# Kernel optimization log

Hardware: AMD Instinct MI355X
Metric: run time of the kernel (lower is better)

Reference implementation:

```python
import jax, jax.numpy as jnp
import numpy as np

N_HEADS = 16
EMBD = 1024
D_HEAD = EMBD // N_HEADS

def setup_inputs() -> dict:
    key = jax.random.key(0)
    ks = jax.random.split(key, 5)
    x = jax.random.normal(ks[0], (2, 2048, EMBD), dtype=jnp.float32)
    # Linear weights stored torch-style [out, in]; apply as x @ W.T + b
    W_in = jax.random.normal(ks[1], (3 * EMBD, EMBD), dtype=jnp.float32) * (EMBD ** -0.5)
    b_in = jax.random.normal(ks[2], (3 * EMBD,), dtype=jnp.float32) * 0.01
    W_out = jax.random.normal(ks[3], (EMBD, EMBD), dtype=jnp.float32) * (EMBD ** -0.5)
    b_out = jax.random.normal(ks[4], (EMBD,), dtype=jnp.float32) * 0.01
    return {"x": x, "W_in": W_in, "b_in": b_in, "W_out": W_out, "b_out": b_out}

def reference(x, W_in, b_in, W_out, b_out):
    B, S, D = x.shape
    qkv = x @ W_in.T + b_in                      # [B, S, 3D]
    q, k, v = jnp.split(qkv, 3, axis=-1)
    def heads(t):
        return t.reshape(B, S, N_HEADS, D_HEAD).transpose(0, 2, 1, 3)  # [B,H,S,d]
    q, k, v = heads(q), heads(k), heads(v)
    scale = 1.0 / jnp.sqrt(jnp.float32(D_HEAD))
    scores = jnp.einsum('bhqd,bhkd->bhqk', q, k) * scale
    weights = jax.nn.softmax(scores, axis=-1)
    out = jnp.einsum('bhqk,bhkd->bhqd', weights, v)  # [B,H,S,d]
    out = out.transpose(0, 2, 1, 3).reshape(B, S, D)
    return out @ W_out.T + b_out
```

## Files before the change

### kernel.cpp

```cpp
#include <hip/hip_runtime.h>
#include <cstdint>

#define EMBD 1024
#define NH 16
#define DH 64
#define BB 2
#define SS 2048
#define M_TOT (BB*SS)
#define N_QKV (3*EMBD)

typedef __bf16 bf16_t;
typedef bf16_t bf16x8 __attribute__((ext_vector_type(8)));
typedef float f32x4 __attribute__((ext_vector_type(4)));
typedef unsigned short u16;
typedef unsigned int u32;

static __device__ __forceinline__ u16 f2bf(float f) {
    union { float f; unsigned u; } c; c.f = f;
    unsigned u = c.u;
    unsigned r = (u + 0x7FFFu + ((u >> 16) & 1u)) >> 16;
    return (u16)r;
}

#define GLDS16(gp, lp) \
    __builtin_amdgcn_global_load_lds((const __attribute__((address_space(1))) void*)(gp), \
                                     (__attribute__((address_space(3))) void*)(lp), 16, 0, 0)

#define NX8 (M_TOT * EMBD / 8)
#define NWI8 (N_QKV * EMBD / 8)
#define NWO8 (EMBD * EMBD / 8)
__global__ void cast_all(const float* __restrict__ x, const float* __restrict__ wi,
                         const float* __restrict__ wo, u16* __restrict__ xb,
                         u16* __restrict__ wib, u16* __restrict__ wob) {
    int i = blockIdx.x * blockDim.x + threadIdx.x;
    const float* s; u16* d; int off;
    if (i < NX8)              { s = x;  d = xb;  off = i; }
    else if (i < NX8 + NWI8)  { s = wi; d = wib; off = i - NX8; }
    else                      { s = wo; d = wob; off = i - NX8 - NWI8; }
    const float4* s4 = (const float4*)s;
    float4 a = s4[2 * off];
    float4 b = s4[2 * off + 1];
    union { u16 u[8]; uint4 v; } r;
    r.u[0] = f2bf(a.x); r.u[1] = f2bf(a.y); r.u[2] = f2bf(a.z); r.u[3] = f2bf(a.w);
    r.u[4] = f2bf(b.x); r.u[5] = f2bf(b.y); r.u[6] = f2bf(b.z); r.u[7] = f2bf(b.w);
    ((uint4*)d)[off] = r.v;
}

#define QSCALE (0.125f * 1.4426950408889634f)
__global__ __launch_bounds__(256) void gemm_qkv(
    const u16* __restrict__ Xb,
    const u16* __restrict__ Wb,
    const float* __restrict__ b_in,
    u16* __restrict__ Q, u16* __restrict__ Kf, u16* __restrict__ Vpf)
{
    __shared__ u16 AB[2][8192];
    const int t = threadIdx.x;
    const int lane = t & 63;
    const int wave = t >> 6;
    const int wm = wave >> 1, wn = wave & 1;
    const int quad = lane >> 4, l16 = lane & 15;
    const int m0 = blockIdx.y * 128, n0 = blockIdx.x * 128;

    const int s0i = t, s1i = 256 + t;
    const u16* ga0 = Xb + (size_t)(m0 + (s0i >> 2)) * EMBD + (s0i & 3) * 8;
    const u16* ga1 = Xb + (size_t)(m0 + (s1i >> 2)) * EMBD + (s1i & 3) * 8;
    const u16* gb0 = Wb + (size_t)(n0 + (s0i >> 2)) * EMBD + (s0i & 3) * 8;
    const u16* gb1 = Wb + (size_t)(n0 + (s1i >> 2)) * EMBD + (s1i & 3) * 8;

    f32x4 acc[4][4] = {};

    {
        u16* buf = &AB[0][0];
        GLDS16(ga0, buf + s0i * 8);
        GLDS16(ga1, buf + s1i * 8);
        GLDS16(gb0, buf + 4096 + s0i * 8);
        GLDS16(gb1, buf + 4096 + s1i * 8);
    }

    for (int it = 0; it < EMBD / 32; ++it) {
        asm volatile("s_waitcnt vmcnt(0)" ::: "memory");
        __syncthreads();
        if (it + 1 < EMBD / 32) {
            int k0 = (it + 1) * 32;
            u16* buf = &AB[(it + 1) & 1][0];
            GLDS16(ga0 + k0, buf + s0i * 8);
            GLDS16(ga1 + k0, buf + s1i * 8);
            GLDS16(gb0 + k0, buf + 4096 + s0i * 8);
            GLDS16(gb1 + k0, buf + 4096 + s1i * 8);
        }
        const u16* As = &AB[it & 1][0];
        const u16* Bs = &AB[it & 1][4096];
        bf16x8 af[4], bfr[4];
#pragma unroll
        for (int im = 0; im < 4; ++im)
            af[im] = *(const bf16x8*)(As + (wm * 64 + im * 16 + l16) * 32 + quad * 8);
#pragma unroll
        for (int in = 0; in < 4; ++in)
            bfr[in] = *(const bf16x8*)(Bs + (wn * 64 + in * 16 + l16) * 32 + quad * 8);
#pragma unroll
        for (int im = 0; im < 4; ++im)
#pragma unroll
            for (int in = 0; in < 4; ++in)
                acc[im][in] = __builtin_amdgcn_mfma_f32_16x16x32_bf16(
                    af[im], bfr[in], acc[im][in], 0, 0, 0);
    }

#pragma unroll
    for (int im = 0; im < 4; ++im) {
        int rbase = m0 + wm * 64 + im * 16 + quad * 4;
        int b = rbase >> 11, ss = rbase & (SS - 1);
#pragma unroll
        for (int in = 0; in < 4; ++in) {
            int col = n0 + wn * 64 + in * 16 + l16;
            float bias = b_in[col];
            float v0 = acc[im][in][0] + bias;
            float v1 = acc[im][in][1] + bias;
            float v2 = acc[im][in][2] + bias;
            float v3 = acc[im][in][3] + bias;
            if (col < EMBD) {
                int h = col >> 6, d = col & 63;
                u16* qp = Q + (((size_t)(b * NH + h) * SS) + ss) * DH + d;
                qp[0]      = f2bf(v0 * QSCALE);
                qp[DH]     = f2bf(v1 * QSCALE);
                qp[2 * DH] = f2bf(v2 * QSCALE);
                qp[3 * DH] = f2bf(v3 * QSCALE);
            } else if (col < 2 * EMBD) {
                int c = col - EMBD; int h = c >> 6, d = c & 63;
                u16* kp = Kf + (size_t)(b * NH + h) * SS * DH
                          + (ss >> 4) * 1024 + (d >> 5) * 512
                          + (ss & 15) * 32 + ((d >> 3) & 3) * 8 + (d & 7);
                kp[0]  = f2bf(v0);
                kp[32] = f2bf(v1);
                kp[64] = f2bf(v2);
                kp[96] = f2bf(v3);
            } else {
                int c = col - 2 * EMBD; int h = c >> 6, d = c & 63;
                int p32 = ((ss >> 2) & 3) * 8 + ((ss >> 4) & 1) * 4;
                u32 lo = (u32)f2bf(v0) | ((u32)f2bf(v1) << 16);
                u32 hi = (u32)f2bf(v2) | ((u32)f2bf(v3) << 16);
                uint2 pk; pk.x = lo; pk.y = hi;
                *(uint2*)(Vpf + (size_t)(b * NH + h) * SS * DH
                          + (ss >> 5) * 2048 + (d >> 4) * 512 + (d & 15) * 32 + p32) = pk;
            }
        }
    }
}

#define OST 72
__global__ __launch_bounds__(256, 2) void attn(
    const u16* __restrict__ Q, const u16* __restrict__ Kf,
    const u16* __restrict__ Vpf, u16* __restrict__ AO)
{
    __shared__ u16 KV[2][8192];
    const int t = threadIdx.x;
    const int lane = t & 63, w = t >> 6;
    const int quad = lane >> 4, l16 = lane & 15;
    const int b0 = blockIdx.x;
    const int bh = (b0 & 7) * 4 + ((b0 >> 3) & 3);
    const int qt = b0 >> 5;
    const int q0 = qt * 128 + w * 32;

    const u16* Qh = Q + ((size_t)bh * SS + q0) * DH;
    const u16* Kh = Kf + (size_t)bh * SS * DH;
    const u16* Vh = Vpf + (size_t)bh * SS * DH;

    bf16x8 qb[2][2];
#pragma unroll
    for (int qi = 0; qi < 2; ++qi) {
        qb[qi][0] = *(const bf16x8*)(Qh + (qi * 16 + l16) * DH + quad * 8);
        qb[qi][1] = *(const bf16x8*)(Qh + (qi * 16 + l16) * DH + 32 + quad * 8);
    }

    f32x4 o[2][4] = {};
    float lsum[2] = {0.f, 0.f};

    GLDS16(Kh + t * 8,        &KV[0][0] + t * 8);
    GLDS16(Kh + 2048 + t * 8, &KV[0][0] + 2048 + t * 8);
    GLDS16(Vh + t * 8,        &KV[0][4096] + t * 8);
    GLDS16(Vh + 2048 + t * 8, &KV[0][4096] + 2048 + t * 8);

    for (int it = 0; it < SS / 64; ++it) {
        asm volatile("s_waitcnt vmcnt(0)" ::: "memory");
        __syncthreads();
        if (it + 1 < SS / 64) {
            const u16* kc = Kh + (it + 1) * 4096;
            const u16* vc = Vh + (it + 1) * 4096;
            u16* kb = &KV[(it + 1) & 1][0];
            u16* vb = &KV[(it + 1) & 1][4096];
            GLDS16(kc + t * 8,        kb + t * 8);
            GLDS16(kc + 2048 + t * 8, kb + 2048 + t * 8);
            GLDS16(vc + t * 8,        vb + t * 8);
            GLDS16(vc + 2048 + t * 8, vb + 2048 + t * 8);
        }
        const u16* Kb = &KV[it & 1][0];
        const u16* Vb = &KV[it & 1][4096];
#pragma unroll
        for (int g = 0; g < 2; ++g) {
            bf16x8 ka00 = *(const bf16x8*)(Kb + (2 * g) * 1024 +       l16 * 32 + quad * 8);
            bf16x8 ka01 = *(const bf16x8*)(Kb + (2 * g) * 1024 + 512 + l16 * 32 + quad * 8);
            bf16x8 ka10 = *(const bf16x8*)(Kb + (2 * g + 1) * 1024 +       l16 * 32 + quad * 8);
            bf16x8 ka11 = *(const bf16x8*)(Kb + (2 * g + 1) * 1024 + 512 + l16 * 32 + quad * 8);
            bf16x8 va0 = *(const bf16x8*)(Vb + g * 2048 +        l16 * 32 + quad * 8);
            bf16x8 va1 = *(const bf16x8*)(Vb + g * 2048 + 512  + l16 * 32 + quad * 8);
            bf16x8 va2 = *(const bf16x8*)(Vb + g * 2048 + 1024 + l16 * 32 + quad * 8);
            bf16x8 va3 = *(const bf16x8*)(Vb + g * 2048 + 1536 + l16 * 32 + quad * 8);
            bf16x8 pb[2];
#pragma unroll
            for (int qi = 0; qi < 2; ++qi) {
                f32x4 z0 = {0.f, 0.f, 0.f, 0.f};
                f32x4 z1 = {0.f, 0.f, 0.f, 0.f};
                z0 = __builtin_amdgcn_mfma_f32_16x16x32_bf16(ka00, qb[qi][0], z0, 0, 0, 0);
                z0 = __builtin_amdgcn_mfma_f32_16x16x32_bf16(ka01, qb[qi][1], z0, 0, 0, 0);
                z1 = __builtin_amdgcn_mfma_f32_16x16x32_bf16(ka10, qb[qi][0], z1, 0, 0, 0);
                z1 = __builtin_amdgcn_mfma_f32_16x16x32_bf16(ka11, qb[qi][1], z1, 0, 0, 0);
                u32 ue[8];
                float ls = 0.f;
#pragma unroll
                for (int j = 0; j < 4; ++j) {
                    float e0 = __builtin_amdgcn_exp2f(z0[j]);
                    float e1 = __builtin_amdgcn_exp2f(z1[j]);
                    ls += e0 + e1;
                    union { float f; u32 v; } c0, c1;
                    c0.f = e0; c1.f = e1;
                    ue[j] = c0.v + 0x8000u;
                    ue[4 + j] = c1.v + 0x8000u;
                }
                lsum[qi] += ls;
                union { uint4 u; bf16x8 b; } cv;
                cv.u.x = __builtin_amdgcn_perm(ue[1], ue[0], 0x07060302u);
                cv.u.y = __builtin_amdgcn_perm(ue[3], ue[2], 0x07060302u);
                cv.u.z = __builtin_amdgcn_perm(ue[5], ue[4], 0x07060302u);
                cv.u.w = __builtin_amdgcn_perm(ue[7], ue[6], 0x07060302u);
                pb[qi] = cv.b;
            }
            o[0][0] = __builtin_amdgcn_mfma_f32_16x16x32_bf16(va0, pb[0], o[0][0], 0, 0, 0);
            o[0][1] = __builtin_amdgcn_mfma_f32_16x16x32_bf16(va1, pb[0], o[0][1], 0, 0, 0);
            o[0][2] = __builtin_amdgcn_mfma_f32_16x16x32_bf16(va2, pb[0], o[0][2], 0, 0, 0);
            o[0][3] = __builtin_amdgcn_mfma_f32_16x16x32_bf16(va3, pb[0], o[0][3], 0, 0, 0);
            o[1][0] = __builtin_amdgcn_mfma_f32_16x16x32_bf16(va0, pb[1], o[1][0], 0, 0, 0);
            o[1][1] = __builtin_amdgcn_mfma_f32_16x16x32_bf16(va1, pb[1], o[1][1], 0, 0, 0);
            o[1][2] = __builtin_amdgcn_mfma_f32_16x16x32_bf16(va2, pb[1], o[1][2], 0, 0, 0);
            o[1][3] = __builtin_amdgcn_mfma_f32_16x16x32_bf16(va3, pb[1], o[1][3], 0, 0, 0);
        }
    }

    float rl[2];
#pragma unroll
    for (int qi = 0; qi < 2; ++qi) {
        float v = lsum[qi];
        v += __shfl_xor(v, 16, 64);
        v += __shfl_xor(v, 32, 64);
        rl[qi] = 1.0f / v;
    }
    __syncthreads();
    u16* Ksc = &KV[0][0];
#pragma unroll
    for (int qi = 0; qi < 2; ++qi)
#pragma unroll
        for (int dt = 0; dt < 4; ++dt)
#pragma unroll
            for (int jj = 0; jj < 2; ++jj) {
                u32 lo_ = (u32)f2bf(o[qi][dt][2 * jj] * rl[qi]);
                u32 hi_ = (u32)f2bf(o[qi][dt][2 * jj + 1] * rl[qi]);
                *(u32*)(Ksc + (w * 32 + qi * 16 + l16) * OST + dt * 16 + quad * 4 + jj * 2) =
                    lo_ | (hi_ << 16);
            }
    __syncthreads();
    const int b = bh >> 4, h = bh & 15;
#pragma unroll
    for (int i = 0; i < 4; ++i) {
        int idx = i * 256 + t;
        int q = idx >> 3, c = idx & 7;
        uint4 vv = *(const uint4*)(Ksc + q * OST + c * 8);
        *(uint4*)(AO + ((size_t)(b * SS + qt * 128 + q)) * EMBD + h * DH + c * 8) = vv;
    }
}

__global__ __launch_bounds__(256) void gemm_out(
    const u16* __restrict__ Ab,
    const u16* __restrict__ Wb,
    const float* __restrict__ b_out,
    float* __restrict__ Out)
{
    __shared__ u16 AB[2][8192];
    const int t = threadIdx.x;
    const int lane = t & 63;
    const int wave = t >> 6;
    const int wm = wave >> 1, wn = wave & 1;
    const int quad = lane >> 4, l16 = lane & 15;
    const int m0 = blockIdx.y * 128, n0 = blockIdx.x * 128;

    const int s0i = t, s1i = 256 + t;
    const u16* ga0 = Ab + (size_t)(m0 + (s0i >> 2)) * EMBD + (s0i & 3) * 8;
    const u16* ga1 = Ab + (size_t)(m0 + (s1i >> 2)) * EMBD + (s1i & 3) * 8;
    const u16* gb0 = Wb + (size_t)(n0 + (s0i >> 2)) * EMBD + (s0i & 3) * 8;
    const u16* gb1 = Wb + (size_t)(n0 + (s1i >> 2)) * EMBD + (s1i & 3) * 8;

    f32x4 acc[4][4] = {};

    {
        u16* buf = &AB[0][0];
        GLDS16(ga0, buf + s0i * 8);
        GLDS16(ga1, buf + s1i * 8);
        GLDS16(gb0, buf + 4096 + s0i * 8);
        GLDS16(gb1, buf + 4096 + s1i * 8);
    }

    for (int it = 0; it < EMBD / 32; ++it) {
        asm volatile("s_waitcnt vmcnt(0)" ::: "memory");
        __syncthreads();
        if (it + 1 < EMBD / 32) {
            int k0 = (it + 1) * 32;
            u16* buf = &AB[(it + 1) & 1][0];
            GLDS16(ga0 + k0, buf + s0i * 8);
            GLDS16(ga1 + k0, buf + s1i * 8);
            GLDS16(gb0 + k0, buf + 4096 + s0i * 8);
            GLDS16(gb1 + k0, buf + 4096 + s1i * 8);
        }
        const u16* As = &AB[it & 1][0];
        const u16* Bs = &AB[it & 1][4096];
        bf16x8 af[4], bfr[4];
#pragma unroll
        for (int im = 0; im < 4; ++im)
            af[im] = *(const bf16x8*)(As + (wm * 64 + im * 16 + l16) * 32 + quad * 8);
#pragma unroll
        for (int in = 0; in < 4; ++in)
            bfr[in] = *(const bf16x8*)(Bs + (wn * 64 + in * 16 + l16) * 32 + quad * 8);
#pragma unroll
        for (int im = 0; im < 4; ++im)
#pragma unroll
            for (int in = 0; in < 4; ++in)
                acc[im][in] = __builtin_amdgcn_mfma_f32_16x16x32_bf16(
                    af[im], bfr[in], acc[im][in], 0, 0, 0);
    }

#pragma unroll
    for (int im = 0; im < 4; ++im) {
        int rbase = m0 + wm * 64 + im * 16 + quad * 4;
#pragma unroll
        for (int in = 0; in < 4; ++in) {
            int col = n0 + wn * 64 + in * 16 + l16;
            float bias = b_out[col];
#pragma unroll
            for (int j = 0; j < 4; ++j)
                Out[(size_t)(rbase + j) * EMBD + col] = acc[im][in][j] + bias;
        }
    }
}

extern "C" void kernel_launch(void* const* d_in, const int* in_sizes, int n_in,
                              void* d_out, int out_size, void* d_ws, size_t ws_size,
                              hipStream_t stream)
{
    (void)in_sizes; (void)n_in; (void)out_size; (void)ws_size;
    const float* x     = (const float*)d_in[0];
    const float* W_in  = (const float*)d_in[1];
    const float* b_in  = (const float*)d_in[2];
    const float* W_out = (const float*)d_in[3];
    const float* b_out = (const float*)d_in[4];
    float* out = (float*)d_out;

    char* ws = (char*)d_ws;
    u16* xb  = (u16*)(ws);
    u16* wib = (u16*)(ws + 8u  * 1024 * 1024);
    u16* wob = (u16*)(ws + 14u * 1024 * 1024);
    u16* Qw  = (u16*)(ws + 16u * 1024 * 1024);
    u16* Kw  = (u16*)(ws + 24u * 1024 * 1024);
    u16* Vpw = (u16*)(ws + 32u * 1024 * 1024);
    u16* AO  = (u16*)(ws + 40u * 1024 * 1024);

    cast_all<<<(NX8 + NWI8 + NWO8) / 256, 256, 0, stream>>>(x, W_in, W_out, xb, wib, wob);
    gemm_qkv<<<dim3(N_QKV / 128, M_TOT / 128), 256, 0, stream>>>(xb, wib, b_in, Qw, Kw, Vpw);
    attn<<<512, 256, 0, stream>>>(Qw, Kw, Vpw, AO);
    gemm_out<<<dim3(EMBD / 128, M_TOT / 128), 256, 0, stream>>>(AO, wob, b_out, out);
}
```

Before: 180.9 us.

## Triple-buffer GEMM loads and double attention KV chunk size

```diff
diff --git a/kernel.cpp b/kernel.cpp
--- a/kernel.cpp
+++ b/kernel.cpp
@@ -53,7 +53,7 @@
     const float* __restrict__ b_in,
     u16* __restrict__ Q, u16* __restrict__ Kf, u16* __restrict__ Vpf)
 {
-    __shared__ u16 AB[2][8192];
+    __shared__ u16 AB[3][8192];
     const int t = threadIdx.x;
     const int lane = t & 63;
     const int wave = t >> 6;
@@ -69,27 +69,30 @@
 
     f32x4 acc[4][4] = {};
 
-    {
-        u16* buf = &AB[0][0];
-        GLDS16(ga0, buf + s0i * 8);
-        GLDS16(ga1, buf + s1i * 8);
-        GLDS16(gb0, buf + 4096 + s0i * 8);
-        GLDS16(gb1, buf + 4096 + s1i * 8);
-    }
-
+#pragma unroll
+    for (int p = 0; p < 2; ++p) {
+        u16* buf = &AB[p][0];
+        GLDS16(ga0 + p * 32, buf + s0i * 8);
+        GLDS16(ga1 + p * 32, buf + s1i * 8);
+        GLDS16(gb0 + p * 32, buf + 4096 + s0i * 8);
+        GLDS16(gb1 + p * 32, buf + 4096 + s1i * 8);
+    }
+
+    int bi = 0;
+    int bw = 2;
     for (int it = 0; it < EMBD / 32; ++it) {
-        asm volatile("s_waitcnt vmcnt(0)" ::: "memory");
+        asm volatile("s_waitcnt vmcnt(4)" ::: "memory");
         __syncthreads();
-        if (it + 1 < EMBD / 32) {
-            int k0 = (it + 1) * 32;
-            u16* buf = &AB[(it + 1) & 1][0];
+        {
+            int k0 = (it + 2) * 32;
+            u16* buf = &AB[bw][0];
             GLDS16(ga0 + k0, buf + s0i * 8);
             GLDS16(ga1 + k0, buf + s1i * 8);
             GLDS16(gb0 + k0, buf + 4096 + s0i * 8);
             GLDS16(gb1 + k0, buf + 4096 + s1i * 8);
         }
-        const u16* As = &AB[it & 1][0];
-        const u16* Bs = &AB[it & 1][4096];
+        const u16* As = &AB[bi][0];
+        const u16* Bs = &AB[bi][4096];
         bf16x8 af[4], bfr[4];
 #pragma unroll
         for (int im = 0; im < 4; ++im)
@@ -103,6 +106,8 @@
             for (int in = 0; in < 4; ++in)
                 acc[im][in] = __builtin_amdgcn_mfma_f32_16x16x32_bf16(
                     af[im], bfr[in], acc[im][in], 0, 0, 0);
+        bi = (bi == 2) ? 0 : bi + 1;
+        bw = (bw == 2) ? 0 : bw + 1;
     }
 
 #pragma unroll
@@ -151,7 +156,7 @@
     const u16* __restrict__ Q, const u16* __restrict__ Kf,
     const u16* __restrict__ Vpf, u16* __restrict__ AO)
 {
-    __shared__ u16 KV[2][8192];
+    __shared__ u16 KV[2][16384];
     const int t = threadIdx.x;
     const int lane = t & 63, w = t >> 6;
     const int quad = lane >> 4, l16 = lane & 15;
@@ -174,28 +179,30 @@
     f32x4 o[2][4] = {};
     float lsum[2] = {0.f, 0.f};
 
-    GLDS16(Kh + t * 8,        &KV[0][0] + t * 8);
-    GLDS16(Kh + 2048 + t * 8, &KV[0][0] + 2048 + t * 8);
-    GLDS16(Vh + t * 8,        &KV[0][4096] + t * 8);
-    GLDS16(Vh + 2048 + t * 8, &KV[0][4096] + 2048 + t * 8);
-
-    for (int it = 0; it < SS / 64; ++it) {
+#pragma unroll
+    for (int i = 0; i < 4; ++i) {
+        GLDS16(Kh + i * 2048 + t * 8, &KV[0][0] + i * 2048 + t * 8);
+        GLDS16(Vh + i * 2048 + t * 8, &KV[0][8192] + i * 2048 + t * 8);
+    }
+
+    for (int it = 0; it < SS / 128; ++it) {
         asm volatile("s_waitcnt vmcnt(0)" ::: "memory");
         __syncthreads();
-        if (it + 1 < SS / 64) {
-            const u16* kc = Kh + (it + 1) * 4096;
-            const u16* vc = Vh + (it + 1) * 4096;
+        if (it + 1 < SS / 128) {
+            const u16* kc = Kh + (it + 1) * 8192;
+            const u16* vc = Vh + (it + 1) * 8192;
             u16* kb = &KV[(it + 1) & 1][0];
-            u16* vb = &KV[(it + 1) & 1][4096];
-            GLDS16(kc + t * 8,        kb + t * 8);
-            GLDS16(kc + 2048 + t * 8, kb + 2048 + t * 8);
-            GLDS16(vc + t * 8,        vb + t * 8);
-            GLDS16(vc + 2048 + t * 8, vb + 2048 + t * 8);
+            u16* vb = &KV[(it + 1) & 1][8192];
+#pragma unroll
+            for (int i = 0; i < 4; ++i) {
+                GLDS16(kc + i * 2048 + t * 8, kb + i * 2048 + t * 8);
+                GLDS16(vc + i * 2048 + t * 8, vb + i * 2048 + t * 8);
+            }
         }
         const u16* Kb = &KV[it & 1][0];
-        const u16* Vb = &KV[it & 1][4096];
-#pragma unroll
-        for (int g = 0; g < 2; ++g) {
+        const u16* Vb = &KV[it & 1][8192];
+#pragma unroll
+        for (int g = 0; g < 4; ++g) {
             bf16x8 ka00 = *(const bf16x8*)(Kb + (2 * g) * 1024 +       l16 * 32 + quad * 8);
             bf16x8 ka01 = *(const bf16x8*)(Kb + (2 * g) * 1024 + 512 + l16 * 32 + quad * 8);
             bf16x8 ka10 = *(const bf16x8*)(Kb + (2 * g + 1) * 1024 +       l16 * 32 + quad * 8);
@@ -282,7 +289,7 @@
     const float* __restrict__ b_out,
     float* __restrict__ Out)
 {
-    __shared__ u16 AB[2][8192];
+    __shared__ u16 AB[3][8192];
     const int t = threadIdx.x;
     const int lane = t & 63;
     const int wave = t >> 6;
@@ -298,27 +305,29 @@
 
     f32x4 acc[4][4] = {};
 
-    {
-        u16* buf = &AB[0][0];
-        GLDS16(ga0, buf + s0i * 8);
-        GLDS16(ga1, buf + s1i * 8);
-        GLDS16(gb0, buf + 4096 + s0i * 8);
-        GLDS16(gb1, buf + 4096 + s1i * 8);
-    }
-
+#pragma unroll
+    for (int p = 0; p < 2; ++p) {
+        u16* buf = &AB[p][0];
+        GLDS16(ga0 + p * 32, buf + s0i * 8);
+        GLDS16(ga1 + p * 32, buf + s1i * 8);
+        GLDS16(gb0 + p * 32, buf + 4096 + s0i * 8);
+        GLDS16(gb1 + p * 32, buf + 4096 + s1i * 8);
+    }
+
+    int bi = 0, bw = 2;
     for (int it = 0; it < EMBD / 32; ++it) {
-        asm volatile("s_waitcnt vmcnt(0)" ::: "memory");
+        asm volatile("s_waitcnt vmcnt(4)" ::: "memory");
         __syncthreads();
-        if (it + 1 < EMBD / 32) {
-            int k0 = (it + 1) * 32;
-            u16* buf = &AB[(it + 1) & 1][0];
+        {
+            int k0 = (it + 2) * 32;
+            u16* buf = &AB[bw][0];
             GLDS16(ga0 + k0, buf + s0i * 8);
             GLDS16(ga1 + k0, buf + s1i * 8);
             GLDS16(gb0 + k0, buf + 4096 + s0i * 8);
             GLDS16(gb1 + k0, buf + 4096 + s1i * 8);
         }
-        const u16* As = &AB[it & 1][0];
-        const u16* Bs = &AB[it & 1][4096];
+        const u16* As = &AB[bi][0];
+        const u16* Bs = &AB[bi][4096];
         bf16x8 af[4], bfr[4];
 #pragma unroll
         for (int im = 0; im < 4; ++im)
@@ -332,6 +341,8 @@
             for (int in = 0; in < 4; ++in)
                 acc[im][in] = __builtin_amdgcn_mfma_f32_16x16x32_bf16(
                     af[im], bfr[in], acc[im][in], 0, 0, 0);
+        bi = (bi == 2) ? 0 : bi + 1;
+        bw = (bw == 2) ? 0 : bw + 1;
     }
 
 #pragma unroll
```

Result: no change. 178.8 us (-1.1%).
